# Kernel optimization log

Measured on AMD Instinct MI355X. Metric: run time of the kernel, lower is better.

Reference implementation:

```python
import jax, jax.numpy as jnp
import numpy as np

B, S, D_IN, D_OUT, H = 4, 2048, 1024, 1024, 16
HD = D_OUT // H  # head_dim = 64


def setup_inputs() -> dict:
    key = jax.random.key(0)
    ks = jax.random.split(key, 7)
    sd_in = 1.0 / np.sqrt(D_IN)
    sd_out = 1.0 / np.sqrt(D_OUT)
    return {
        "x": jax.random.normal(ks[0], (B, S, D_IN), dtype=jnp.float32),
        # weights stored [in, out] so y = x @ W (equivalent to torch Linear)
        "wq": jax.random.uniform(ks[1], (D_IN, D_OUT), jnp.float32, -sd_in, sd_in),
        "wk": jax.random.uniform(ks[2], (D_IN, D_OUT), jnp.float32, -sd_in, sd_in),
        "wv": jax.random.uniform(ks[3], (D_IN, D_OUT), jnp.float32, -sd_in, sd_in),
        "wo": jax.random.uniform(ks[4], (D_OUT, D_OUT), jnp.float32, -sd_out, sd_out),
        "bo": jax.random.uniform(ks[5], (D_OUT,), jnp.float32, -sd_out, sd_out),
    }


def reference(x, wq, wk, wv, wo, bo):
    b, n, _ = x.shape
    # project and split heads: [b, h, n, hd]
    q = (x @ wq).reshape(b, n, H, HD).transpose(0, 2, 1, 3)
    k = (x @ wk).reshape(b, n, H, HD).transpose(0, 2, 1, 3)
    v = (x @ wv).reshape(b, n, H, HD).transpose(0, 2, 1, 3)
    scale = 1.0 / jnp.sqrt(jnp.asarray(HD, dtype=x.dtype))
    scores = jnp.einsum('bhqd,bhkd->bhqk', q, k) * scale  # [b,h,n,n]
    causal = jnp.tril(jnp.ones((n, n), dtype=bool))
    scores = jnp.where(causal, scores, -jnp.inf)
    attn = jax.nn.softmax(scores, axis=-1)
    # dropout p=0.0 -> identity
    ctx = jnp.einsum('bhqk,bhkd->bhqd', attn, v)
    ctx = ctx.transpose(0, 2, 1, 3).reshape(b, n, D_OUT)
    return ctx @ wo + bo
```

## Files before the change

kernel.cpp:

```cpp
#include <hip/hip_runtime.h>

#define DEVINL __device__ __forceinline__

typedef __attribute__((ext_vector_type(8))) short s8v;
typedef __attribute__((ext_vector_type(4))) float f4v;
typedef __attribute__((ext_vector_type(16))) float f16v;
typedef __attribute__((ext_vector_type(8))) __bf16 bf8v;
typedef __attribute__((ext_vector_type(4))) unsigned int u4v;

static constexpr int SEQ = 2048;
static constexpr int DIM = 1024;
static constexpr int NH = 16;

DEVINL unsigned short f2bf(float f) {
  unsigned int u = __builtin_bit_cast(unsigned int, f);
  u += 0x7FFFu + ((u >> 16) & 1u);
  return (unsigned short)(u >> 16);
}

DEVINL void gl_lds16(const void* g, void* l) {
  __builtin_amdgcn_global_load_lds((__attribute__((address_space(1))) void*)g,
                                   (__attribute__((address_space(3))) void*)l,
                                   16, 0, 0);
}

DEVINL f4v mfma16(s8v a, s8v b, f4v c) {
  return __builtin_amdgcn_mfma_f32_16x16x32_bf16(__builtin_bit_cast(bf8v, a),
                                                 __builtin_bit_cast(bf8v, b),
                                                 c, 0, 0, 0);
}

DEVINL f16v mfma32(s8v a, s8v b, f16v c) {
  return __builtin_amdgcn_mfma_f32_32x32x16_bf16(__builtin_bit_cast(bf8v, a),
                                                 __builtin_bit_cast(bf8v, b),
                                                 c, 0, 0, 0);
}

DEVINL unsigned cvtpk(float lo, float hi) {
  unsigned r;
  asm("v_cvt_pk_bf16_f32 %0, %1, %2" : "=v"(r) : "v"(lo), "v"(hi));
  return r;
}

DEVINL void plswap(unsigned& a, unsigned& b) {
#if __has_builtin(__builtin_amdgcn_permlane32_swap)
  typedef int i2v __attribute__((ext_vector_type(2)));
  i2v r = __builtin_amdgcn_permlane32_swap((int)a, (int)b, false, false);
  a = (unsigned)r[0]; b = (unsigned)r[1];
#else
  asm volatile("v_permlane32_swap_b32 %0, %1" : "+v"(a), "+v"(b));
#endif
}

DEVINL s8v mkfrag(unsigned w0, unsigned w1, unsigned w2, unsigned w3) {
  u4v t = {w0, w1, w2, w3};
  return __builtin_bit_cast(s8v, t);
}

__global__ __launch_bounds__(256) void k_cvt(const float* __restrict__ in,
                                             unsigned short* __restrict__ outp) {
  const int i = blockIdx.x * 256 + threadIdx.x;
  const f4v* p = (const f4v*)in + (size_t)i * 2;
  f4v a = p[0], b = p[1];
  s8v o;
  o[0] = (short)f2bf(a[0]); o[1] = (short)f2bf(a[1]);
  o[2] = (short)f2bf(a[2]); o[3] = (short)f2bf(a[3]);
  o[4] = (short)f2bf(b[0]); o[5] = (short)f2bf(b[1]);
  o[6] = (short)f2bf(b[2]); o[7] = (short)f2bf(b[3]);
  ((s8v*)outp)[i] = o;
}

__global__ __launch_bounds__(256) void k_twt(const float* __restrict__ w0, const float* __restrict__ w1,
                                             const float* __restrict__ w2, const float* __restrict__ w3,
                                             unsigned short* __restrict__ o0, unsigned short* __restrict__ o1,
                                             unsigned short* __restrict__ o2, unsigned short* __restrict__ o3) {
  __shared__ float tile[32][33];
  const float* w = blockIdx.z == 0 ? w0 : blockIdx.z == 1 ? w1 : blockIdx.z == 2 ? w2 : w3;
  unsigned short* o = blockIdx.z == 0 ? o0 : blockIdx.z == 1 ? o1 : blockIdx.z == 2 ? o2 : o3;
  const int r0 = blockIdx.y * 32, c0 = blockIdx.x * 32;
  const int tx = threadIdx.x & 31, ty = threadIdx.x >> 5;
#pragma unroll
  for (int i = 0; i < 32; i += 8) tile[ty + i][tx] = w[(r0 + ty + i) * DIM + c0 + tx];
  __syncthreads();
#pragma unroll
  for (int i = 0; i < 32; i += 8) o[(c0 + ty + i) * DIM + r0 + tx] = f2bf(tile[tx][ty + i]);
}

DEVINL void gemm_loop(const unsigned short* __restrict__ A, const unsigned short* __restrict__ Bt,
                      int m0, int n0, char* As, char* Bs, f4v acc[4][4]) {
  const int tid = threadIdx.x;
  const int lane = tid & 63;
  const int l15 = lane & 15, lg = lane >> 4;
  const int wm = (tid >> 6) >> 1, wn = (tid >> 6) & 1;
  for (int k0 = 0; k0 < 1024; k0 += 64) {
    __syncthreads();
#pragma unroll
    for (int i = 0; i < 4; ++i) {
      const int c = i * 256 + tid;
      const int row = c >> 3;
      const int csw = ((c & 7) ^ (row & 7)) * 8;
      gl_lds16(A + (size_t)(m0 + row) * 1024 + k0 + csw, As + c * 16);
      gl_lds16(Bt + (size_t)(n0 + row) * 1024 + k0 + csw, Bs + c * 16);
    }
    __syncthreads();
#pragma unroll
    for (int kk = 0; kk < 2; ++kk) {
      s8v af[4], bfr[4];
      const int kb2 = (kk * 32 + lg * 8) * 2;
#pragma unroll
      for (int mf = 0; mf < 4; ++mf) {
        const int row = wm * 64 + mf * 16 + l15;
        af[mf] = *(const s8v*)(As + row * 128 + (kb2 ^ ((row & 7) << 4)));
      }
#pragma unroll
      for (int nf = 0; nf < 4; ++nf) {
        const int row = wn * 64 + nf * 16 + l15;
        bfr[nf] = *(const s8v*)(Bs + row * 128 + (kb2 ^ ((row & 7) << 4)));
      }
#pragma unroll
      for (int mf = 0; mf < 4; ++mf)
#pragma unroll
        for (int nf = 0; nf < 4; ++nf) acc[mf][nf] = mfma16(af[mf], bfr[nf], acc[mf][nf]);
    }
  }
}

__global__ __launch_bounds__(256) void k_qkv(const unsigned short* __restrict__ xb,
                                             const unsigned short* __restrict__ wqt,
                                             const unsigned short* __restrict__ wkt,
                                             const unsigned short* __restrict__ wvt,
                                             unsigned short* __restrict__ q,
                                             unsigned short* __restrict__ k,
                                             unsigned short* __restrict__ v) {
  __shared__ __align__(16) char smem[32768];
  const int m0 = blockIdx.x * 128;
  const int which = blockIdx.y >> 3;
  const int n0 = (blockIdx.y & 7) * 128;
  const unsigned short* Bt = which == 0 ? wqt : which == 1 ? wkt : wvt;
  unsigned short* C = which == 0 ? q : which == 1 ? k : v;
  const float oscale = which == 0 ? 0.125f * 1.44269504f : 1.0f;
  f4v acc[4][4];
  f4v z = {0.f, 0.f, 0.f, 0.f};
#pragma unroll
  for (int a = 0; a < 4; ++a)
#pragma unroll
    for (int b = 0; b < 4; ++b) acc[a][b] = z;
  gemm_loop(xb, Bt, m0, n0, smem, smem + 16384, acc);
  const int lane = threadIdx.x & 63;
  const int l15 = lane & 15, lg = lane >> 4;
  const int wm = (threadIdx.x >> 6) >> 1, wn = (threadIdx.x >> 6) & 1;
#pragma unroll
  for (int mf = 0; mf < 4; ++mf)
#pragma unroll
    for (int nf = 0; nf < 4; ++nf)
#pragma unroll
      for (int r = 0; r < 4; ++r) {
        const int row = m0 + wm * 64 + mf * 16 + lg * 4 + r;
        const int col = n0 + wn * 64 + nf * 16 + l15;
        C[(size_t)row * 1024 + col] = f2bf(acc[mf][nf][r] * oscale);
      }
}

__global__ __launch_bounds__(256) void k_oproj(const unsigned short* __restrict__ ctx,
                                               const unsigned short* __restrict__ wot,
                                               const float* __restrict__ bo,
                                               float* __restrict__ outp) {
  __shared__ __align__(16) char smem[32768];
  const int m0 = blockIdx.x * 128, n0 = blockIdx.y * 128;
  f4v acc[4][4];
  f4v z = {0.f, 0.f, 0.f, 0.f};
#pragma unroll
  for (int a = 0; a < 4; ++a)
#pragma unroll
    for (int b = 0; b < 4; ++b) acc[a][b] = z;
  gemm_loop(ctx, wot, m0, n0, smem, smem + 16384, acc);
  const int lane = threadIdx.x & 63;
  const int l15 = lane & 15, lg = lane >> 4;
  const int wm = (threadIdx.x >> 6) >> 1, wn = (threadIdx.x >> 6) & 1;
#pragma unroll
  for (int nf = 0; nf < 4; ++nf) {
    const int col = n0 + wn * 64 + nf * 16 + l15;
    const float bias = bo[col];
#pragma unroll
    for (int mf = 0; mf < 4; ++mf)
#pragma unroll
      for (int r = 0; r < 4; ++r) {
        const int row = m0 + wm * 64 + mf * 16 + lg * 4 + r;
        outp[(size_t)row * 1024 + col] = acc[mf][nf][r] + bias;
      }
  }
}

__global__ __launch_bounds__(256) void k_tv(const unsigned short* __restrict__ v,
                                            unsigned short* __restrict__ vt) {
  __shared__ unsigned short tile[64][65];
  const int b = blockIdx.z, h = blockIdx.y, s0 = blockIdx.x * 64;
  const int t = threadIdx.x;
#pragma unroll
  for (int i = 0; i < 16; ++i) {
    const int s = i * 4 + (t >> 6), d = t & 63;
    tile[s][d] = v[(size_t)(b * SEQ + s0 + s) * 1024 + h * 64 + d];
  }
  __syncthreads();
#pragma unroll
  for (int i = 0; i < 16; ++i) {
    const int d = i * 4 + (t >> 6), s = t & 63;
    vt[(size_t)((b * NH + h) * 64 + d) * SEQ + s0 + s] = tile[s][d];
  }
}

DEVINL void stage_kv(const unsigned short* __restrict__ kbase,
                     const unsigned short* __restrict__ vbase,
                     int kv0, char* Ks, char* Vs, int tid) {
#pragma unroll
  for (int i = 0; i < 2; ++i) {
    const int c = i * 256 + tid;
    const int row = c >> 3;
    const int csw = ((c & 7) ^ (row & 7)) * 8;
    gl_lds16(kbase + (size_t)(kv0 + row) * 1024 + csw, Ks + c * 16);
    gl_lds16(vbase + (size_t)row * SEQ + kv0 + csw, Vs + c * 16);
  }
}

__global__ __launch_bounds__(256) void k_attn(const unsigned short* __restrict__ q,
                                              const unsigned short* __restrict__ kg,
                                              const unsigned short* __restrict__ vt,
                                              unsigned short* __restrict__ ctx) {
  __shared__ __align__(16) char smem[32768];
  const int b = blockIdx.z, h = blockIdx.y, pair = blockIdx.x;
  const int tid = threadIdx.x, lane = tid & 63, w = tid >> 6;
  const int l31 = lane & 31, hi = lane >> 5;

  const unsigned short* kbase = kg + (size_t)b * SEQ * 1024 + h * 64;
  const unsigned short* vbase = vt + (size_t)((b * NH + h) * 64) * SEQ;

  f16v z16;
#pragma unroll
  for (int i = 0; i < 16; ++i) z16[i] = 0.f;

  for (int seg = 0; seg < 2; ++seg) {
    const int qi = seg == 0 ? pair : 15 - pair;
    const int qbb = qi * 128;
    const int qg = qbb + w * 32 + l31;
    const unsigned short* qp = q + (size_t)(b * SEQ + qg) * 1024 + h * 64;
    s8v qf[4];
#pragma unroll
    for (int kd = 0; kd < 4; ++kd) qf[kd] = *(const s8v*)(qp + kd * 16 + hi * 8);

    f16v o0 = z16, o1 = z16;
    float m = -3e38f, lsum = 0.f;
    const int nt = qi * 2 + 2;

    __syncthreads();
    stage_kv(kbase, vbase, 0, smem, smem + 16384, tid);

    for (int t = 0; t < nt; ++t) {
      const int kv0 = t * 64;
      char* Ks = smem + (t & 1) * 8192;
      char* Vs = smem + 16384 + (t & 1) * 8192;
      __syncthreads();
      if (t + 1 < nt)
        stage_kv(kbase, vbase, kv0 + 64, smem + ((t + 1) & 1) * 8192,
                 smem + 16384 + ((t + 1) & 1) * 8192, tid);
      if (kv0 > qbb + w * 32 + 31) continue;

      f16v s0 = z16, s1 = z16;
#pragma unroll
      for (int kd = 0; kd < 4; ++kd) {
        const int off = kd * 32 + hi * 16;
        const int r0 = l31, r1 = 32 + l31;
        const s8v kf0 = *(const s8v*)(Ks + r0 * 128 + (off ^ ((r0 & 7) << 4)));
        const s8v kf1 = *(const s8v*)(Ks + r1 * 128 + (off ^ ((r1 & 7) << 4)));
        s0 = mfma32(kf0, qf[kd], s0);
        s1 = mfma32(kf1, qf[kd], s1);
      }

      const bool needmask = (kv0 + 63 > qbb + w * 32);
      const int crel = qg - kv0;
      float tmax = -3e38f;
#pragma unroll
      for (int r = 0; r < 16; ++r) {
        const int kvloc = (r & 3) + 8 * (r >> 2) + 4 * hi;
        float v0 = s0[r], v1 = s1[r];
        if (needmask) {
          if (kvloc > crel) v0 = -3e38f;
          if (kvloc + 32 > crel) v1 = -3e38f;
        }
        s0[r] = v0; s1[r] = v1;
        tmax = fmaxf(tmax, fmaxf(v0, v1));
      }
      tmax = fmaxf(tmax, __shfl_xor(tmax, 32));

      const bool grew = tmax > m + 8.f;
      const float mnew = grew ? tmax : m;
      const float corr = __builtin_amdgcn_exp2f(m - mnew);
      m = mnew;

      float rs = 0.f;
#pragma unroll
      for (int r = 0; r < 16; ++r) {
        const float e0 = __builtin_amdgcn_exp2f(s0[r] - m);
        const float e1 = __builtin_amdgcn_exp2f(s1[r] - m);
        s0[r] = e0; s1[r] = e1;
        rs += e0 + e1;
      }
      rs += __shfl_xor(rs, 32);
      lsum = lsum * corr + rs;
      if (__any(grew)) { o0 *= corr; o1 *= corr; }

      unsigned a0 = cvtpk(s0[0], s0[1]), b0 = cvtpk(s0[4], s0[5]); plswap(a0, b0);
      unsigned a1 = cvtpk(s0[2], s0[3]), b1 = cvtpk(s0[6], s0[7]); plswap(a1, b1);
      const s8v f0 = mkfrag(a0, a1, b0, b1);
      unsigned a2 = cvtpk(s0[8], s0[9]), b2 = cvtpk(s0[12], s0[13]); plswap(a2, b2);
      unsigned a3 = cvtpk(s0[10], s0[11]), b3 = cvtpk(s0[14], s0[15]); plswap(a3, b3);
      const s8v f1 = mkfrag(a2, a3, b2, b3);
      unsigned a4 = cvtpk(s1[0], s1[1]), b4 = cvtpk(s1[4], s1[5]); plswap(a4, b4);
      unsigned a5 = cvtpk(s1[2], s1[3]), b5 = cvtpk(s1[6], s1[7]); plswap(a5, b5);
      const s8v f2 = mkfrag(a4, a5, b4, b5);
      unsigned a6 = cvtpk(s1[8], s1[9]), b6 = cvtpk(s1[12], s1[13]); plswap(a6, b6);
      unsigned a7 = cvtpk(s1[10], s1[11]), b7 = cvtpk(s1[14], s1[15]); plswap(a7, b7);
      const s8v f3 = mkfrag(a6, a7, b6, b7);

#pragma unroll
      for (int ks = 0; ks < 4; ++ks) {
        const s8v pb = ks == 0 ? f0 : ks == 1 ? f1 : ks == 2 ? f2 : f3;
        const int off = ks * 32 + hi * 16;
        const int rd0 = l31, rd1 = 32 + l31;
        const s8v v0 = *(const s8v*)(Vs + rd0 * 128 + (off ^ ((rd0 & 7) << 4)));
        const s8v v1 = *(const s8v*)(Vs + rd1 * 128 + (off ^ ((rd1 & 7) << 4)));
        o0 = mfma32(v0, pb, o0);
        o1 = mfma32(v1, pb, o1);
      }
    }

    const float rl = 1.f / lsum;
    unsigned short* crow_p = ctx + (size_t)(b * SEQ + qg) * 1024 + h * 64;
#pragma unroll
    for (int r = 0; r < 16; ++r) {
      const int d = (r & 3) + 8 * (r >> 2) + 4 * hi;
      crow_p[d] = f2bf(o0[r] * rl);
      crow_p[32 + d] = f2bf(o1[r] * rl);
    }
  }
}

extern "C" void kernel_launch(void* const* d_in, const int* in_sizes, int n_in,
                              void* d_out, int out_size, void* d_ws, size_t ws_size,
                              hipStream_t stream) {
  (void)in_sizes; (void)n_in; (void)out_size; (void)ws_size;
  const float* x = (const float*)d_in[0];
  const float* wq = (const float*)d_in[1];
  const float* wk = (const float*)d_in[2];
  const float* wv = (const float*)d_in[3];
  const float* wo = (const float*)d_in[4];
  const float* bo = (const float*)d_in[5];
  float* outp = (float*)d_out;
  char* ws = (char*)d_ws;
  const size_t MB = 1ull << 20;
  unsigned short* xb  = (unsigned short*)(ws + 0 * MB);
  unsigned short* wqt = (unsigned short*)(ws + 16 * MB);
  unsigned short* wkt = (unsigned short*)(ws + 18 * MB);
  unsigned short* wvt = (unsigned short*)(ws + 20 * MB);
  unsigned short* wot = (unsigned short*)(ws + 22 * MB);
  unsigned short* qb_ = (unsigned short*)(ws + 24 * MB);
  unsigned short* kb_ = (unsigned short*)(ws + 40 * MB);
  unsigned short* vb_ = (unsigned short*)(ws + 56 * MB);
  unsigned short* vtb = (unsigned short*)(ws + 72 * MB);
  unsigned short* ctx = (unsigned short*)(ws + 88 * MB);

  k_cvt<<<4096, 256, 0, stream>>>(x, xb);
  k_twt<<<dim3(32, 32, 4), 256, 0, stream>>>(wq, wk, wv, wo, wqt, wkt, wvt, wot);
  k_qkv<<<dim3(64, 24), 256, 0, stream>>>(xb, wqt, wkt, wvt, qb_, kb_, vb_);
  k_tv<<<dim3(32, 16, 4), 256, 0, stream>>>(vb_, vtb);
  k_attn<<<dim3(8, 16, 4), 256, 0, stream>>>(qb_, kb_, vtb, ctx);
  k_oproj<<<dim3(64, 8), 256, 0, stream>>>(ctx, wot, bo, outp);
}
```

Baseline: 260.6 us.

## Double-buffer GEMM K-loop with async LDS loads and remap workgroups across XCDs

Replaces the single-buffer GEMM loop in the QKV and output projections with a two-stage LDS ring. The next K tile is loaded via global_load_lds while the current one is computed, with explicit vmcnt waits and barriers, so load latency is hidden behind MFMA work. Block indices are also remapped so consecutive workgroups on the same XCD share A/B tiles for better L2 reuse. LDS per block doubles to 64KB, which may lower occupancy.

```diff
diff --git a/kernel.cpp b/kernel.cpp
--- a/kernel.cpp
+++ b/kernel.cpp
@@ -86,43 +86,67 @@
   for (int i = 0; i < 32; i += 8) o[(c0 + ty + i) * DIM + r0 + tx] = f2bf(tile[tx][ty + i]);
 }
 
-DEVINL void gemm_loop(const unsigned short* __restrict__ A, const unsigned short* __restrict__ Bt,
-                      int m0, int n0, char* As, char* Bs, f4v acc[4][4]) {
+DEVINL void stage128(const unsigned short* __restrict__ A, const unsigned short* __restrict__ Bt,
+                     int m0, int n0, int k0, char* Ab, char* Bb, int tid) {
+#pragma unroll
+  for (int ld = 0; ld < 4; ++ld) {
+    const int c = ld * 256 + tid;
+    const int row = c >> 3;
+    const int csw = ((c & 7) ^ (row & 7)) * 8;
+    gl_lds16(A + (size_t)(m0 + row) * 1024 + k0 + csw, Ab + c * 16);
+    gl_lds16(Bt + (size_t)(n0 + row) * 1024 + k0 + csw, Bb + c * 16);
+  }
+}
+
+DEVINL void gemm_compute_tile(char* Ar, char* Br, f4v acc[4][4],
+                              int l15, int lg, int wm, int wn) {
+#pragma unroll
+  for (int kk = 0; kk < 2; ++kk) {
+    s8v af[4], bfr[4];
+    const int kb2 = (kk * 32 + lg * 8) * 2;
+#pragma unroll
+    for (int mf = 0; mf < 4; ++mf) {
+      const int row = wm * 64 + mf * 16 + l15;
+      af[mf] = *(const s8v*)(Ar + row * 128 + (kb2 ^ ((row & 7) << 4)));
+    }
+#pragma unroll
+    for (int nf = 0; nf < 4; ++nf) {
+      const int row = wn * 64 + nf * 16 + l15;
+      bfr[nf] = *(const s8v*)(Br + row * 128 + (kb2 ^ ((row & 7) << 4)));
+    }
+#pragma unroll
+    for (int mf = 0; mf < 4; ++mf)
+#pragma unroll
+      for (int nf = 0; nf < 4; ++nf) acc[mf][nf] = mfma16(af[mf], bfr[nf], acc[mf][nf]);
+  }
+}
+
+DEVINL void gemm_ring(const unsigned short* __restrict__ A, const unsigned short* __restrict__ Bt,
+                      int m0, int n0, char* smem, f4v acc[4][4]) {
   const int tid = threadIdx.x;
-  const int lane = tid & 63;
-  const int l15 = lane & 15, lg = lane >> 4;
+  const int lane = tid & 63, l15 = lane & 15, lg = lane >> 4;
   const int wm = (tid >> 6) >> 1, wn = (tid >> 6) & 1;
-  for (int k0 = 0; k0 < 1024; k0 += 64) {
-    __syncthreads();
-#pragma unroll
-    for (int i = 0; i < 4; ++i) {
-      const int c = i * 256 + tid;
-      const int row = c >> 3;
-      const int csw = ((c & 7) ^ (row & 7)) * 8;
-      gl_lds16(A + (size_t)(m0 + row) * 1024 + k0 + csw, As + c * 16);
-      gl_lds16(Bt + (size_t)(n0 + row) * 1024 + k0 + csw, Bs + c * 16);
-    }
-    __syncthreads();
-#pragma unroll
-    for (int kk = 0; kk < 2; ++kk) {
-      s8v af[4], bfr[4];
-      const int kb2 = (kk * 32 + lg * 8) * 2;
-#pragma unroll
-      for (int mf = 0; mf < 4; ++mf) {
-        const int row = wm * 64 + mf * 16 + l15;
-        af[mf] = *(const s8v*)(As + row * 128 + (kb2 ^ ((row & 7) << 4)));
-      }
-#pragma unroll
-      for (int nf = 0; nf < 4; ++nf) {
-        const int row = wn * 64 + nf * 16 + l15;
-        bfr[nf] = *(const s8v*)(Bs + row * 128 + (kb2 ^ ((row & 7) << 4)));
-      }
-#pragma unroll
-      for (int mf = 0; mf < 4; ++mf)
-#pragma unroll
-        for (int nf = 0; nf < 4; ++nf) acc[mf][nf] = mfma16(af[mf], bfr[nf], acc[mf][nf]);
-    }
-  }
+  constexpr int NT = 16;
+
+  stage128(A, Bt, m0, n0, 0, smem, smem + 32768, tid);
+
+  for (int t = 0; t < NT - 1; ++t) {
+    const int nb = (t + 1) & 1;
+    stage128(A, Bt, m0, n0, (t + 1) * 64, smem + nb * 16384, smem + 32768 + nb * 16384, tid);
+    asm volatile("s_waitcnt vmcnt(8)" ::: "memory");
+    __builtin_amdgcn_s_barrier();
+    __builtin_amdgcn_sched_barrier(0);
+    const int cb = t & 1;
+    gemm_compute_tile(smem + cb * 16384, smem + 32768 + cb * 16384, acc, l15, lg, wm, wn);
+    asm volatile("s_waitcnt lgkmcnt(0)" ::: "memory");
+    __builtin_amdgcn_sched_barrier(0);
+    __builtin_amdgcn_s_barrier();
+  }
+  asm volatile("s_waitcnt vmcnt(0)" ::: "memory");
+  __builtin_amdgcn_s_barrier();
+  __builtin_amdgcn_sched_barrier(0);
+  gemm_compute_tile(smem + ((NT - 1) & 1) * 16384, smem + 32768 + ((NT - 1) & 1) * 16384,
+                    acc, l15, lg, wm, wn);
 }
 
 __global__ __launch_bounds__(256) void k_qkv(const unsigned short* __restrict__ xb,
@@ -132,22 +156,23 @@
                                              unsigned short* __restrict__ q,
                                              unsigned short* __restrict__ k,
                                              unsigned short* __restrict__ v) {
-  __shared__ __align__(16) char smem[32768];
-  const int m0 = blockIdx.x * 128;
-  const int which = blockIdx.y >> 3;
-  const int n0 = (blockIdx.y & 7) * 128;
+  __shared__ __align__(16) char smem[65536];
+  const int wgid = (blockIdx.x & 7) * 192 + (blockIdx.x >> 3);
+  const int m0 = (wgid / 24) * 128;
+  const int rem = wgid % 24;
+  const int which = rem >> 3;
+  const int n0 = (rem & 7) * 128;
   const unsigned short* Bt = which == 0 ? wqt : which == 1 ? wkt : wvt;
   unsigned short* C = which == 0 ? q : which == 1 ? k : v;
   const float oscale = which == 0 ? 0.125f * 1.44269504f : 1.0f;
   f4v acc[4][4];
-  f4v z = {0.f, 0.f, 0.f, 0.f};
+  const f4v z = {0.f, 0.f, 0.f, 0.f};
 #pragma unroll
   for (int a = 0; a < 4; ++a)
 #pragma unroll
     for (int b = 0; b < 4; ++b) acc[a][b] = z;
-  gemm_loop(xb, Bt, m0, n0, smem, smem + 16384, acc);
-  const int lane = threadIdx.x & 63;
-  const int l15 = lane & 15, lg = lane >> 4;
+  gemm_ring(xb, Bt, m0, n0, smem, acc);
+  const int lane = threadIdx.x & 63, l15 = lane & 15, lg = lane >> 4;
   const int wm = (threadIdx.x >> 6) >> 1, wn = (threadIdx.x >> 6) & 1;
 #pragma unroll
   for (int mf = 0; mf < 4; ++mf)
@@ -165,17 +190,18 @@
                                                const unsigned short* __restrict__ wot,
                                                const float* __restrict__ bo,
                                                float* __restrict__ outp) {
-  __shared__ __align__(16) char smem[32768];
-  const int m0 = blockIdx.x * 128, n0 = blockIdx.y * 128;
+  __shared__ __align__(16) char smem[65536];
+  const int wgid = (blockIdx.x & 7) * 64 + (blockIdx.x >> 3);
+  const int m0 = (wgid >> 3) * 128;
+  const int n0 = (wgid & 7) * 128;
   f4v acc[4][4];
-  f4v z = {0.f, 0.f, 0.f, 0.f};
+  const f4v z = {0.f, 0.f, 0.f, 0.f};
 #pragma unroll
   for (int a = 0; a < 4; ++a)
 #pragma unroll
     for (int b = 0; b < 4; ++b) acc[a][b] = z;
-  gemm_loop(ctx, wot, m0, n0, smem, smem + 16384, acc);
-  const int lane = threadIdx.x & 63;
-  const int l15 = lane & 15, lg = lane >> 4;
+  gemm_ring(ctx, wot, m0, n0, smem, acc);
+  const int lane = threadIdx.x & 63, l15 = lane & 15, lg = lane >> 4;
   const int wm = (threadIdx.x >> 6) >> 1, wn = (threadIdx.x >> 6) & 1;
 #pragma unroll
   for (int nf = 0; nf < 4; ++nf) {
@@ -370,8 +396,8 @@
 
   k_cvt<<<4096, 256, 0, stream>>>(x, xb);
   k_twt<<<dim3(32, 32, 4), 256, 0, stream>>>(wq, wk, wv, wo, wqt, wkt, wvt, wot);
-  k_qkv<<<dim3(64, 24), 256, 0, stream>>>(xb, wqt, wkt, wvt, qb_, kb_, vb_);
+  k_qkv<<<1536, 256, 0, stream>>>(xb, wqt, wkt, wvt, qb_, kb_, vb_);
   k_tv<<<dim3(32, 16, 4), 256, 0, stream>>>(vb_, vtb);
   k_attn<<<dim3(8, 16, 4), 256, 0, stream>>>(qb_, kb_, vtb, ctx);
-  k_oproj<<<dim3(64, 8), 256, 0, stream>>>(ctx, wot, bo, outp);
-}
+  k_oproj<<<512, 256, 0, stream>>>(ctx, wot, bo, outp);
+}
```

After: 256.1 us. No clear change (-1.7%).
